# Kernel tuning notes

Hardware: AMD Instinct MI355X
Metric: run time of the kernel (lower is better)

The kernel has to match this reference:

```python
import jax, jax.numpy as jnp
import numpy as np

N_NODES = 50000
N_EDGES = 1600000
IN_FEATURES = 128
D_ATT = 64
N_HEADS = 8
D_HEAD = D_ATT // N_HEADS
EPS = 1e-16  # torch_geometric softmax eps


def setup_inputs() -> dict:
    key = jax.random.key(0)
    ks = jax.random.split(key, 9)
    return {
        "x": jax.random.normal(ks[0], (N_NODES, IN_FEATURES), dtype=jnp.float32),
        "Wq": jax.random.normal(ks[1], (D_ATT, IN_FEATURES), dtype=jnp.float32) * 0.02,
        "bq": jax.random.normal(ks[2], (D_ATT,), dtype=jnp.float32) * 0.02,
        "Wk": jax.random.normal(ks[3], (D_ATT, IN_FEATURES), dtype=jnp.float32) * 0.02,
        "bk": jax.random.normal(ks[4], (D_ATT,), dtype=jnp.float32) * 0.02,
        "Wv": jax.random.normal(ks[5], (D_ATT, IN_FEATURES), dtype=jnp.float32) * 0.02,
        "bv": jax.random.normal(ks[6], (D_ATT,), dtype=jnp.float32) * 0.02,
        "edge_attr": jax.random.uniform(ks[7], (N_EDGES,), dtype=jnp.float32),
        "edge": jax.random.randint(ks[8], (2, N_EDGES), 0, N_NODES, dtype=jnp.int64),
    }


def segment_softmax(logits, seg, num_segments):
    # logits: (E, H), seg: (E,) destination-node ids
    m = jax.ops.segment_max(logits, seg, num_segments=num_segments)  # (N, H)
    ex = jnp.exp(logits - m[seg])
    s = jax.ops.segment_sum(ex, seg, num_segments=num_segments)      # (N, H)
    return ex / (s[seg] + EPS)


def reference(x, Wq, bq, Wk, bk, Wv, bv, edge_attr, edge):
    n = x.shape[0]
    # Linear projections, reshape to (N, n_heads, d_head) then transpose(1,2) -> (N, d_head, n_heads)
    q = (x @ Wq.T + bq).reshape(n, N_HEADS, D_HEAD).transpose(0, 2, 1)
    k = (x @ Wk.T + bk).reshape(n, N_HEADS, D_HEAD).transpose(0, 2, 1)
    v = (x @ Wv.T + bv).reshape(n, N_HEADS, D_HEAD).transpose(0, 2, 1)
    src = q[edge[0]]     # (E, d_head, n_heads)
    dst_k = k[edge[1]]   # (E, d_head, n_heads)
    prods = jnp.sum(src * dst_k, axis=1) / np.sqrt(D_HEAD).astype(np.float32)  # (E, n_heads)
    # reweight_attention=True with per-edge scalar edge_attr
    prods = prods * edge_attr[:, None]
    # square_plus=False -> segment softmax grouped by edge[attention_norm_idx=1]
    attention = segment_softmax(prods, edge[1], N_NODES)
    return attention, v, prods
```

## Files before the change

kernel.cpp:

```cpp
#include <hip/hip_runtime.h>
#include <hip/hip_bf16.h>
#include <math.h>

#define N_NODES   50000
#define N_EDGES   1600000
#define IN_F      128
#define D_ATT     64
#define N_HEADS   8
#define D_HEAD    8
#define RSQRT8    0.35355339059327373f
#define EPS_SM    1e-16f
#define NEH       (N_EDGES * N_HEADS)

typedef float f32x4 __attribute__((ext_vector_type(4)));

__device__ inline unsigned short f2bf(float v) {
    __hip_bfloat16 b = __float2bfloat16(v);
    return *(unsigned short*)&b;
}
__device__ inline float bflo(unsigned u) { return __uint_as_float(u << 16); }
__device__ inline float bfhi(unsigned u) { return __uint_as_float(u & 0xffff0000u); }

__global__ __launch_bounds__(256) void k_proj(
        const float* __restrict__ x,
        const float* __restrict__ Wq, const float* __restrict__ bq,
        const float* __restrict__ Wk, const float* __restrict__ bk,
        const float* __restrict__ Wv, const float* __restrict__ bv,
        unsigned short* __restrict__ qp, unsigned short* __restrict__ kp,
        float* __restrict__ vout, float* __restrict__ s) {
    __shared__ float Xs[128][64];
    __shared__ float Ws[128][64];
    const int tid = threadIdx.x;
    const int n0  = blockIdx.x * 64;
    const int ln  = tid & 63;
    const int kb  = tid >> 6;

    {
        int nthr = gridDim.x * 256;
        for (int i = blockIdx.x * 256 + tid; i < N_NODES * N_HEADS; i += nthr)
            s[i] = 0.0f;
    }

    {
        int n = n0 + ln;
        if (n < N_NODES) {
            const float4* xr = (const float4*)(x + (size_t)n * IN_F + kb * 32);
#pragma unroll
            for (int i = 0; i < 8; ++i) {
                float4 v = xr[i];
                int k = kb * 32 + i * 4;
                Xs[k + 0][ln] = v.x; Xs[k + 1][ln] = v.y;
                Xs[k + 2][ln] = v.z; Xs[k + 3][ln] = v.w;
            }
        } else {
#pragma unroll
            for (int i = 0; i < 8; ++i) {
                int k = kb * 32 + i * 4;
                Xs[k + 0][ln] = 0.f; Xs[k + 1][ln] = 0.f;
                Xs[k + 2][ln] = 0.f; Xs[k + 3][ln] = 0.f;
            }
        }
    }

    const int tx = tid & 15;
    const int ty = tid >> 4;

    const float* Wlist[3] = {Wq, Wk, Wv};
    const float* blist[3] = {bq, bk, bv};

    for (int mm = 0; mm < 3; ++mm) {
        __syncthreads();
        {
            const float4* wr = (const float4*)(Wlist[mm] + (size_t)ln * IN_F + kb * 32);
#pragma unroll
            for (int i = 0; i < 8; ++i) {
                float4 v = wr[i];
                int k = kb * 32 + i * 4;
                Ws[k + 0][ln] = v.x; Ws[k + 1][ln] = v.y;
                Ws[k + 2][ln] = v.z; Ws[k + 3][ln] = v.w;
            }
        }
        __syncthreads();

        float acc[4][4] = {};
#pragma unroll 4
        for (int kk = 0; kk < 128; ++kk) {
            float4 a = *(const float4*)&Xs[kk][tx * 4];
            float4 b = *(const float4*)&Ws[kk][ty * 4];
            float xr[4] = {a.x, a.y, a.z, a.w};
            float wr[4] = {b.x, b.y, b.z, b.w};
#pragma unroll
            for (int i = 0; i < 4; ++i)
#pragma unroll
                for (int j = 0; j < 4; ++j)
                    acc[i][j] += xr[i] * wr[j];
        }

        float bj[4];
#pragma unroll
        for (int j = 0; j < 4; ++j) bj[j] = blist[mm][ty * 4 + j];

#pragma unroll
        for (int i = 0; i < 4; ++i) {
            int nn = n0 + tx * 4 + i;
            if (nn >= N_NODES) continue;
            if (mm < 2) {
                unsigned short* dstp = (mm == 0 ? qp : kp) + (size_t)nn * 64 + ty * 4;
                ushort4 o;
                o.x = f2bf(acc[i][0] + bj[0]);
                o.y = f2bf(acc[i][1] + bj[1]);
                o.z = f2bf(acc[i][2] + bj[2]);
                o.w = f2bf(acc[i][3] + bj[3]);
                *(ushort4*)dstp = o;
            } else {
#pragma unroll
                for (int j = 0; j < 4; ++j) {
                    int jj = ty * 4 + j;
                    vout[(size_t)nn * 64 + (jj & 7) * 8 + (jj >> 3)] =
                        acc[i][j] + bj[j];
                }
            }
        }
    }
}

__global__ void k_prods_exp(const int* __restrict__ e0, const int* __restrict__ e1,
                            const float* __restrict__ ea,
                            const unsigned short* __restrict__ qp,
                            const unsigned short* __restrict__ kp,
                            float* __restrict__ prods_out,
                            float* __restrict__ s) {
    int t = blockIdx.x * blockDim.x + threadIdx.x;
    if (t >= NEH) return;
    int e = t >> 3, h = t & 7;
    int src = e0[e];
    int dst = e1[e];
    float w = ea[e] * RSQRT8;
    uint4 qv = *(const uint4*)(qp + (size_t)src * 64 + h * 8);
    uint4 kv = *(const uint4*)(kp + (size_t)dst * 64 + h * 8);
    float dot = bflo(qv.x) * bflo(kv.x) + bfhi(qv.x) * bfhi(kv.x)
              + bflo(qv.y) * bflo(kv.y) + bfhi(qv.y) * bfhi(kv.y)
              + bflo(qv.z) * bflo(kv.z) + bfhi(qv.z) * bfhi(kv.z)
              + bflo(qv.w) * bflo(kv.w) + bfhi(qv.w) * bfhi(kv.w);
    float p = dot * w;
    __builtin_nontemporal_store(p, &prods_out[t]);
    atomicAdd(&s[(size_t)dst * 8 + h], __expf(p));
}

__global__ void k_norm(const int* __restrict__ e1,
                       const float* __restrict__ prods,
                       float* __restrict__ att,
                       const float* __restrict__ s) {
    int i = blockIdx.x * blockDim.x + threadIdx.x;
    if (i >= NEH / 4) return;
    int e  = i >> 1;
    int h0 = (i & 1) * 4;
    int dst = e1[e];

    f32x4 pv = __builtin_nontemporal_load(&((const f32x4*)prods)[i]);
    f32x4 sv = *(const f32x4*)(s + (size_t)dst * 8 + h0);

    f32x4 a;
    a.x = __expf(pv.x) / (sv.x + EPS_SM);
    a.y = __expf(pv.y) / (sv.y + EPS_SM);
    a.z = __expf(pv.z) / (sv.z + EPS_SM);
    a.w = __expf(pv.w) / (sv.w + EPS_SM);
    __builtin_nontemporal_store(a, &((f32x4*)att)[i]);
}

extern "C" void kernel_launch(void* const* d_in, const int* in_sizes, int n_in,
                              void* d_out, int out_size, void* d_ws, size_t ws_size,
                              hipStream_t stream) {
    const float* x  = (const float*)d_in[0];
    const float* Wq = (const float*)d_in[1];
    const float* bq = (const float*)d_in[2];
    const float* Wk = (const float*)d_in[3];
    const float* bk = (const float*)d_in[4];
    const float* Wv = (const float*)d_in[5];
    const float* bv = (const float*)d_in[6];
    const float* ea = (const float*)d_in[7];
    const int*   edge = (const int*)d_in[8];
    const int* e0 = edge;
    const int* e1 = edge + N_EDGES;

    float* out   = (float*)d_out;
    float* att   = out;
    float* vout  = att + (size_t)NEH;
    float* prods = vout + (size_t)N_NODES * D_ATT;

    unsigned short* qp = (unsigned short*)d_ws;
    unsigned short* kp = qp + (size_t)N_NODES * D_ATT;
    float* ssum = (float*)(kp + (size_t)N_NODES * D_ATT);

    const int B = 256;
    int nTiles = (N_NODES + 63) / 64;
    k_proj<<<nTiles, 256, 0, stream>>>(x, Wq, bq, Wk, bk, Wv, bv,
                                       qp, kp, vout, ssum);

    int nEH = NEH;
    k_prods_exp<<<(nEH + B - 1) / B, B, 0, stream>>>(e0, e1, ea, qp, kp,
                                                     prods, ssum);

    int nV = NEH / 4;
    k_norm<<<(nV + B - 1) / B, B, 0, stream>>>(e1, prods, att, ssum);
}
```

Measured before the change: 300.6 us.

## Pack two heads' exp sums into fixed-point 64-bit atomics, two heads per thread

Each edge thread now handles two heads and accumulates both softmax denominators with one 64-bit integer atomicAdd. The exp values are converted to 2^21-scaled fixed-point and packed into two 32-bit halves, and the sum buffer is laid out head-pair-major. This halves the number of atomic operations and threads, and integer atomics may be cheaper than float atomics. The cost is quantization error in the sums and possible overflow of a 32-bit half if a node's exp sum exceeds about 2048, which would carry into the adjacent head's sum.

```diff
diff --git a/kernel.cpp b/kernel.cpp
--- a/kernel.cpp
+++ b/kernel.cpp
@@ -11,8 +11,12 @@
 #define RSQRT8    0.35355339059327373f
 #define EPS_SM    1e-16f
 #define NEH       (N_EDGES * N_HEADS)
+#define NE4       (N_EDGES * 4)
+#define SFIX      2097152.0f
+#define SFIX_INV  (1.0f / 2097152.0f)
 
 typedef float f32x4 __attribute__((ext_vector_type(4)));
+typedef float f32x2 __attribute__((ext_vector_type(2)));
 
 __device__ inline unsigned short f2bf(float v) {
     __hip_bfloat16 b = __float2bfloat16(v);
@@ -20,6 +24,13 @@
 }
 __device__ inline float bflo(unsigned u) { return __uint_as_float(u << 16); }
 __device__ inline float bfhi(unsigned u) { return __uint_as_float(u & 0xffff0000u); }
+
+__device__ inline float dot8(uint4 a, uint4 b) {
+    return bflo(a.x) * bflo(b.x) + bfhi(a.x) * bfhi(b.x)
+         + bflo(a.y) * bflo(b.y) + bfhi(a.y) * bfhi(b.y)
+         + bflo(a.z) * bflo(b.z) + bfhi(a.z) * bfhi(b.z)
+         + bflo(a.w) * bflo(b.w) + bfhi(a.w) * bfhi(b.w);
+}
 
 __global__ __launch_bounds__(256) void k_proj(
         const float* __restrict__ x,
@@ -27,7 +38,7 @@
         const float* __restrict__ Wk, const float* __restrict__ bk,
         const float* __restrict__ Wv, const float* __restrict__ bv,
         unsigned short* __restrict__ qp, unsigned short* __restrict__ kp,
-        float* __restrict__ vout, float* __restrict__ s) {
+        float* __restrict__ vout, unsigned long long* __restrict__ s64) {
     __shared__ float Xs[128][64];
     __shared__ float Ws[128][64];
     const int tid = threadIdx.x;
@@ -37,8 +48,8 @@
 
     {
         int nthr = gridDim.x * 256;
-        for (int i = blockIdx.x * 256 + tid; i < N_NODES * N_HEADS; i += nthr)
-            s[i] = 0.0f;
+        for (int i = blockIdx.x * 256 + tid; i < N_NODES * 4; i += nthr)
+            s64[i] = 0ULL;
     }
 
     {
@@ -124,47 +135,62 @@
     }
 }
 
-__global__ void k_prods_exp(const int* __restrict__ e0, const int* __restrict__ e1,
-                            const float* __restrict__ ea,
-                            const unsigned short* __restrict__ qp,
-                            const unsigned short* __restrict__ kp,
-                            float* __restrict__ prods_out,
-                            float* __restrict__ s) {
+__global__ void k_edge(const int* __restrict__ e0, const int* __restrict__ e1,
+                       const float* __restrict__ ea,
+                       const unsigned short* __restrict__ qp,
+                       const unsigned short* __restrict__ kp,
+                       float* __restrict__ prods_out,
+                       unsigned long long* __restrict__ s64) {
     int t = blockIdx.x * blockDim.x + threadIdx.x;
-    if (t >= NEH) return;
-    int e = t >> 3, h = t & 7;
+    if (t >= NE4) return;
+    int e = t >> 2, l = t & 3;
     int src = e0[e];
     int dst = e1[e];
     float w = ea[e] * RSQRT8;
-    uint4 qv = *(const uint4*)(qp + (size_t)src * 64 + h * 8);
-    uint4 kv = *(const uint4*)(kp + (size_t)dst * 64 + h * 8);
-    float dot = bflo(qv.x) * bflo(kv.x) + bfhi(qv.x) * bfhi(kv.x)
-              + bflo(qv.y) * bflo(kv.y) + bfhi(qv.y) * bfhi(kv.y)
-              + bflo(qv.z) * bflo(kv.z) + bfhi(qv.z) * bfhi(kv.z)
-              + bflo(qv.w) * bflo(kv.w) + bfhi(qv.w) * bfhi(kv.w);
-    float p = dot * w;
-    __builtin_nontemporal_store(p, &prods_out[t]);
-    atomicAdd(&s[(size_t)dst * 8 + h], __expf(p));
+
+    const unsigned short* qr = qp + (size_t)src * 64 + l * 16;
+    const unsigned short* kr = kp + (size_t)dst * 64 + l * 16;
+    uint4 qa = *(const uint4*)qr;
+    uint4 qb = *(const uint4*)(qr + 8);
+    uint4 ka = *(const uint4*)kr;
+    uint4 kb = *(const uint4*)(kr + 8);
+
+    float p0 = dot8(qa, ka) * w;
+    float p1 = dot8(qb, kb) * w;
+
+    f32x2 pv; pv.x = p0; pv.y = p1;
+    __builtin_nontemporal_store(pv, (f32x2*)(prods_out + (size_t)e * 8 + l * 2));
+
+    unsigned u0 = (unsigned)(__expf(p0) * SFIX + 0.5f);
+    unsigned u1 = (unsigned)(__expf(p1) * SFIX + 0.5f);
+    unsigned long long pack = (unsigned long long)u0
+                            | ((unsigned long long)u1 << 32);
+    atomicAdd(&s64[(size_t)l * N_NODES + dst], pack);
 }
 
 __global__ void k_norm(const int* __restrict__ e1,
                        const float* __restrict__ prods,
                        float* __restrict__ att,
-                       const float* __restrict__ s) {
+                       const unsigned long long* __restrict__ s64) {
     int i = blockIdx.x * blockDim.x + threadIdx.x;
     if (i >= NEH / 4) return;
     int e  = i >> 1;
-    int h0 = (i & 1) * 4;
+    int l0 = (i & 1) * 2;
     int dst = e1[e];
 
+    unsigned long long u0 = s64[(size_t)l0 * N_NODES + dst];
+    unsigned long long u1 = s64[(size_t)(l0 + 1) * N_NODES + dst];
+    float s0 = (float)(unsigned)(u0)       * SFIX_INV;
+    float s1 = (float)(unsigned)(u0 >> 32) * SFIX_INV;
+    float s2 = (float)(unsigned)(u1)       * SFIX_INV;
+    float s3 = (float)(unsigned)(u1 >> 32) * SFIX_INV;
+
     f32x4 pv = __builtin_nontemporal_load(&((const f32x4*)prods)[i]);
-    f32x4 sv = *(const f32x4*)(s + (size_t)dst * 8 + h0);
-
     f32x4 a;
-    a.x = __expf(pv.x) / (sv.x + EPS_SM);
-    a.y = __expf(pv.y) / (sv.y + EPS_SM);
-    a.z = __expf(pv.z) / (sv.z + EPS_SM);
-    a.w = __expf(pv.w) / (sv.w + EPS_SM);
+    a.x = __expf(pv.x) / (s0 + EPS_SM);
+    a.y = __expf(pv.y) / (s1 + EPS_SM);
+    a.z = __expf(pv.z) / (s2 + EPS_SM);
+    a.w = __expf(pv.w) / (s3 + EPS_SM);
     __builtin_nontemporal_store(a, &((f32x4*)att)[i]);
 }
 
@@ -190,17 +216,17 @@
 
     unsigned short* qp = (unsigned short*)d_ws;
     unsigned short* kp = qp + (size_t)N_NODES * D_ATT;
-    float* ssum = (float*)(kp + (size_t)N_NODES * D_ATT);
+    unsigned long long* s64 =
+        (unsigned long long*)(kp + (size_t)N_NODES * D_ATT);
 
     const int B = 256;
     int nTiles = (N_NODES + 63) / 64;
     k_proj<<<nTiles, 256, 0, stream>>>(x, Wq, bq, Wk, bk, Wv, bv,
-                                       qp, kp, vout, ssum);
-
-    int nEH = NEH;
-    k_prods_exp<<<(nEH + B - 1) / B, B, 0, stream>>>(e0, e1, ea, qp, kp,
-                                                     prods, ssum);
+                                       qp, kp, vout, s64);
+
+    k_edge<<<(NE4 + B - 1) / B, B, 0, stream>>>(e0, e1, ea, qp, kp,
+                                                prods, s64);
 
     int nV = NEH / 4;
-    k_norm<<<(nV + B - 1) / B, B, 0, stream>>>(e1, prods, att, ssum);
-}
+    k_norm<<<(nV + B - 1) / B, B, 0, stream>>>(e1, prods, att, s64);
+}
```

After: 513.8 us. 70.9% more time.
